# Kernel tuning notes

Measured on AMD Instinct MI355X. Metric: run time of the kernel, lower is better.

## Reference

```python
import jax, jax.numpy as jnp
import numpy as np

EPS = 1e-5


def _conv1x1(x, w, b=None):
    # x: [B,Cin,H,W], w: [Cout,Cin]
    y = jnp.einsum('bchw,oc->bohw', x, w)
    return y if b is None else y + b[None, :, None, None]


def _bn(x, g, bt, m, v):
    # inference-mode BatchNorm2d
    s = g / jnp.sqrt(v + EPS)
    return x * s[None, :, None, None] + (bt - m * s)[None, :, None, None]


def _emb(x, p):
    h = jax.nn.gelu(_conv1x1(x, p['emb_w1'], p['emb_b1']), approximate=False)
    return _conv1x1(h, p['emb_w2'], p['emb_b2'])  # dropout is identity in eval


def _forward(x0, x1, p):
    b, c, h, w = x0.shape
    hw = h * w
    half = c // 2
    xs = [x0, x1]
    la_res = None
    for k in range(4):
        # residual refinement of each scale
        for i in range(2):
            r = _conv1x1(xs[i], p['rb_w1'], p['rb_b1'])
            r = jax.nn.relu(_bn(r, p['rb_bn_g'], p['rb_bn_b'], p['rb_bn_m'], p['rb_bn_v']))
            r = _conv1x1(r, p['rb_w2'], p['rb_b2'])
            xs[i] = jax.nn.relu(_bn(xs[i] + r, p['bn_g'], p['bn_b'], p['bn_m'], p['bn_v']))
        # build per-pixel query [b,hw,half,4] and value [b,hw,4,half]
        qs, vs = [], []
        for i in range(2):
            q = _bn(_conv1x1(xs[i], p['q_w'], p['q_b']), p['q_bn_g'], p['q_bn_b'], p['q_bn_m'], p['q_bn_v'])
            qs += [q[:, :half], q[:, half:]]
            v = _bn(_conv1x1(xs[i], p['v_w'], p['v_b']), p['v_bn_g'], p['v_bn_b'], p['v_bn_m'], p['v_bn_v'])
            vs += [v[:, :half], v[:, half:]]
        query = jnp.stack(qs, axis=1).reshape(b, 4, half, hw).transpose(0, 3, 2, 1)
        value = jnp.stack(vs, axis=1).reshape(b, 4, half, hw).transpose(0, 3, 1, 2)
        if k == 0:
            cat = jnp.concatenate(xs, axis=1)
            la_res = jax.nn.relu(_bn(_conv1x1(cat, p['cf_w'], p['cf_b']),
                                     p['cf_bn_g'], p['cf_bn_b'], p['cf_bn_m'], p['cf_bn_v']))
            la_res = _emb(la_res, p)
        refs = []
        for pref in ('k1', 'k2'):
            kk = _bn(_conv1x1(la_res, p[pref + '_w'], p[pref + '_b']),
                     p[pref + '_bn_g'], p[pref + '_bn_b'], p[pref + '_bn_m'], p[pref + '_bn_v'])
            kk = kk.reshape(b, half, hw).transpose(0, 2, 1)            # [b,hw,half]
            att = jax.nn.softmax(jnp.einsum('bnc,bncm->bnm', kk, query), axis=-1)  # [b,hw,4]
            ref = jnp.einsum('bnm,bnmc->bnc', att, value)               # [b,hw,half]
            refs.append(ref.transpose(0, 2, 1).reshape(b, half, h, w))
        la_res = _emb(jnp.concatenate(refs, axis=1), p)
    return la_res


def setup_inputs() -> dict:
    b, c, h, w = 16, 48, 128, 128
    half = c // 2
    ks = iter(jax.random.split(jax.random.key(0), 64))
    def nrm(shape, s=1.0):
        return s * jax.random.normal(next(ks), shape, jnp.float32)
    inp = {'x0': nrm((b, c, h, w)), 'x1': nrm((b, c, h, w))}
    def conv(wn, bname, o, i):
        inp[wn] = nrm((o, i), 1.0 / np.sqrt(i))
        inp[bname] = nrm((o,), 0.02)
    def bnp(pref, n):
        inp[pref + '_g'] = 1.0 + nrm((n,), 0.1)
        inp[pref + '_b'] = nrm((n,), 0.1)
        inp[pref + '_m'] = nrm((n,), 0.1)
        inp[pref + '_v'] = 1.0 + 0.1 * jnp.abs(nrm((n,)))
    conv('rb_w1', 'rb_b1', half, c); bnp('rb_bn', half)
    conv('rb_w2', 'rb_b2', c, half); bnp('bn', c)
    conv('q_w', 'q_b', c, c); bnp('q_bn', c)
    conv('v_w', 'v_b', c, c); bnp('v_bn', c)
    conv('k1_w', 'k1_b', half, c); bnp('k1_bn', half)
    conv('k2_w', 'k2_b', half, c); bnp('k2_bn', half)
    conv('cf_w', 'cf_b', c, 2 * c); bnp('cf_bn', c)
    conv('emb_w1', 'emb_b1', half, c)
    conv('emb_w2', 'emb_b2', c, half)
    return inp


def reference(x0, x1, rb_w1, rb_b1, rb_bn_g, rb_bn_b, rb_bn_m, rb_bn_v, rb_w2, rb_b2,
              bn_g, bn_b, bn_m, bn_v, q_w, q_b, q_bn_g, q_bn_b, q_bn_m, q_bn_v,
              v_w, v_b, v_bn_g, v_bn_b, v_bn_m, v_bn_v,
              k1_w, k1_b, k1_bn_g, k1_bn_b, k1_bn_m, k1_bn_v,
              k2_w, k2_b, k2_bn_g, k2_bn_b, k2_bn_m, k2_bn_v,
              cf_w, cf_b, cf_bn_g, cf_bn_b, cf_bn_m, cf_bn_v,
              emb_w1, emb_b1, emb_w2, emb_b2):
    p = dict(rb_w1=rb_w1, rb_b1=rb_b1, rb_bn_g=rb_bn_g, rb_bn_b=rb_bn_b, rb_bn_m=rb_bn_m, rb_bn_v=rb_bn_v,
             rb_w2=rb_w2, rb_b2=rb_b2, bn_g=bn_g, bn_b=bn_b, bn_m=bn_m, bn_v=bn_v,
             q_w=q_w, q_b=q_b, q_bn_g=q_bn_g, q_bn_b=q_bn_b, q_bn_m=q_bn_m, q_bn_v=q_bn_v,
             v_w=v_w, v_b=v_b, v_bn_g=v_bn_g, v_bn_b=v_bn_b, v_bn_m=v_bn_m, v_bn_v=v_bn_v,
             k1_w=k1_w, k1_b=k1_b, k1_bn_g=k1_bn_g, k1_bn_b=k1_bn_b, k1_bn_m=k1_bn_m, k1_bn_v=k1_bn_v,
             k2_w=k2_w, k2_b=k2_b, k2_bn_g=k2_bn_g, k2_bn_b=k2_bn_b, k2_bn_m=k2_bn_m, k2_bn_v=k2_bn_v,
             cf_w=cf_w, cf_b=cf_b, cf_bn_g=cf_bn_g, cf_bn_b=cf_bn_b, cf_bn_m=cf_bn_m, cf_bn_v=cf_bn_v,
             emb_w1=emb_w1, emb_b1=emb_b1, emb_w2=emb_w2, emb_b2=emb_b2)
    return _forward(x0, x1, p)
```

## Files before the change

### kernel.cpp

```cpp
#include <hip/hip_runtime.h>
#include <hip/hip_fp16.h>
#include <stdint.h>
#include <math.h>

#define HWS 16384
#define NPIX (16 * HWS)
#define T 256

typedef _Float16 h2 __attribute__((ext_vector_type(2)));

enum {
  H_W1P = 0,
  F_B1  = 576,
  H_W2P = 600,
  F_B2  = 1176,
  F_XS  = 1224,
  H_M1A = 1272,
  H_M1B = 1848,
  H_M2A = 2424,
  H_M2B = 3000,
  F_C1A = 3576, F_C1B = 3624, F_C2A = 3672, F_C2B = 3720,
  F_D1A = 3768, F_D1B = 3792, F_D2A = 3816, F_D2B = 3840,
  F_E4  = 3864,
  H_P1  = 3868,
  H_P2  = 5020,
  F_Q1L = 6172, F_Q1H = 6196, F_Q2L = 6220, F_Q2H = 6244,
  F_BE1 = 6268,
  F_CFT = 6292,
  F_BCF = 10900,
  F_WE1 = 10948,
  F_BE2 = 12100,
  F_WE2R= 12148,
  WS_TOTAL = 13300
};

struct PtrPack { const float* p[48]; };

__device__ __forceinline__ void bnst(const PtrPack& P, int bnb, int o, float& s, float& t) {
  float g = P.p[bnb][o], be = P.p[bnb + 1][o], m = P.p[bnb + 2][o], v = P.p[bnb + 3][o];
  s = g / sqrtf(v + 1e-5f);
  t = be - m * s;
}
__device__ __forceinline__ float KFv(const PtrPack& P, const float* kw, int bnb, int ok, int j) {
  float s, t; bnst(P, bnb, ok, s, t);
  float a = 0.f;
  for (int cc = 0; cc < 48; cc++) a += kw[ok * 48 + cc] * P.p[46][cc * 24 + j];
  return s * a;
}
__device__ __forceinline__ float BFv(const PtrPack& P, const float* kw, const float* kb, int bnb, int ok) {
  float s, t; bnst(P, bnb, ok, s, t);
  float a = kb[ok];
  for (int cc = 0; cc < 48; cc++) a += kw[ok * 48 + cc] * P.p[47][cc];
  return s * a + t;
}
__device__ __forceinline__ float WQf(const PtrPack& P, int o, int c) { float s, t; bnst(P, 16, o, s, t); return s * P.p[14][o * 48 + c]; }
__device__ __forceinline__ float BQf(const PtrPack& P, int o) { float s, t; bnst(P, 16, o, s, t); return s * P.p[15][o] + t; }
__device__ __forceinline__ float WVf(const PtrPack& P, int o, int c) { float s, t; bnst(P, 22, o, s, t); return s * P.p[20][o * 48 + c]; }
__device__ __forceinline__ float BVf(const PtrPack& P, int o) { float s, t; bnst(P, 22, o, s, t); return s * P.p[21][o] + t; }

__device__ float w1v(const PtrPack& P, int c, int o) { float s, t; bnst(P, 4, o, s, t); return s * P.p[2][o * 48 + c]; }
__device__ float w2v(const PtrPack& P, int o, int c) { float s, t; bnst(P, 10, o, s, t); return s * P.p[8][o * 24 + c]; }
__device__ float m_v(const PtrPack& P, int which, int c, int j) {
  float a = 0.f;
  if (which == 0)      for (int ok = 0; ok < 24; ok++) a += KFv(P, P.p[26], 28, ok, j) * WQf(P, ok, c);
  else if (which == 1) for (int ok = 0; ok < 24; ok++) a += KFv(P, P.p[26], 28, ok, j) * WQf(P, 24 + ok, c);
  else if (which == 2) for (int ok = 0; ok < 24; ok++) a += KFv(P, P.p[32], 34, ok, j) * WQf(P, ok, c);
  else                 for (int ok = 0; ok < 24; ok++) a += KFv(P, P.p[32], 34, ok, j) * WQf(P, 24 + ok, c);
  return a;
}
__device__ float p_v(const PtrPack& P, int which, int c, int o) {
  float a = 0.f;
  if (which == 0)      for (int jj = 0; jj < 24; jj++) a += P.p[44][o * 48 + jj] * WVf(P, jj, c);
  else if (which == 1) for (int jj = 0; jj < 24; jj++) a += P.p[44][o * 48 + jj] * WVf(P, 24 + jj, c);
  else if (which == 2) for (int jj = 0; jj < 24; jj++) a += P.p[44][o * 48 + 24 + jj] * WVf(P, jj, c);
  else                 for (int jj = 0; jj < 24; jj++) a += P.p[44][o * 48 + 24 + jj] * WVf(P, 24 + jj, c);
  return a;
}

__device__ __forceinline__ float packh2(float a, float b) {
  __half2 h = __floats2half2_rn(a, b);
  union { __half2 h; float f; } x; x.h = h; return x.f;
}

__global__ void fold_kernel(PtrPack P, float* __restrict__ W) {
  int i = blockIdx.x * blockDim.x + threadIdx.x;
  if (i >= WS_TOTAL) return;
  float s, t, a;
  if (i < F_B1)        { int cp = i / 24, o = i % 24; W[i] = packh2(w1v(P, 2 * cp, o), w1v(P, 2 * cp + 1, o)); }
  else if (i < H_W2P)  { int o = i - F_B1; bnst(P, 4, o, s, t); W[i] = s * P.p[3][o] + t; }
  else if (i < F_B2)   { int j = i - H_W2P; int o = j / 12, cj = j % 12; W[i] = packh2(w2v(P, o, 2 * cj), w2v(P, o, 2 * cj + 1)); }
  else if (i < F_XS)   { int o = i - F_B2; bnst(P, 10, o, s, t); W[i] = s * P.p[9][o] + t; }
  else if (i < H_M1A)  { int o = i - F_XS; bnst(P, 10, o, s, t); W[i] = s; }
  else if (i < H_M1B)  { int j = i - H_M1A; int c = j / 12, jp = j % 12; W[i] = packh2(m_v(P, 0, c, 2 * jp), m_v(P, 0, c, 2 * jp + 1)); }
  else if (i < H_M2A)  { int j = i - H_M1B; int c = j / 12, jp = j % 12; W[i] = packh2(m_v(P, 1, c, 2 * jp), m_v(P, 1, c, 2 * jp + 1)); }
  else if (i < H_M2B)  { int j = i - H_M2A; int c = j / 12, jp = j % 12; W[i] = packh2(m_v(P, 2, c, 2 * jp), m_v(P, 2, c, 2 * jp + 1)); }
  else if (i < F_C1A)  { int j = i - H_M2B; int c = j / 12, jp = j % 12; W[i] = packh2(m_v(P, 3, c, 2 * jp), m_v(P, 3, c, 2 * jp + 1)); }
  else if (i < F_C1B)  { int c = i - F_C1A; a = 0.f; for (int ok = 0; ok < 24; ok++) a += BFv(P, P.p[26], P.p[27], 28, ok) * WQf(P, ok, c); W[i] = a; }
  else if (i < F_C2A)  { int c = i - F_C1B; a = 0.f; for (int ok = 0; ok < 24; ok++) a += BFv(P, P.p[26], P.p[27], 28, ok) * WQf(P, 24 + ok, c); W[i] = a; }
  else if (i < F_C2B)  { int c = i - F_C2A; a = 0.f; for (int ok = 0; ok < 24; ok++) a += BFv(P, P.p[32], P.p[33], 34, ok) * WQf(P, ok, c); W[i] = a; }
  else if (i < F_D1A)  { int c = i - F_C2B; a = 0.f; for (int ok = 0; ok < 24; ok++) a += BFv(P, P.p[32], P.p[33], 34, ok) * WQf(P, 24 + ok, c); W[i] = a; }
  else if (i < F_D1B)  { int j = i - F_D1A; a = 0.f; for (int ok = 0; ok < 24; ok++) a += KFv(P, P.p[26], 28, ok, j) * BQf(P, ok); W[i] = a; }
  else if (i < F_D2A)  { int j = i - F_D1B; a = 0.f; for (int ok = 0; ok < 24; ok++) a += KFv(P, P.p[26], 28, ok, j) * BQf(P, 24 + ok); W[i] = a; }
  else if (i < F_D2B)  { int j = i - F_D2A; a = 0.f; for (int ok = 0; ok < 24; ok++) a += KFv(P, P.p[32], 34, ok, j) * BQf(P, ok); W[i] = a; }
  else if (i < F_E4)   { int j = i - F_D2B; a = 0.f; for (int ok = 0; ok < 24; ok++) a += KFv(P, P.p[32], 34, ok, j) * BQf(P, 24 + ok); W[i] = a; }
  else if (i < H_P1)   { int e = i - F_E4; a = 0.f;
    if (e == 0)      for (int ok = 0; ok < 24; ok++) a += BFv(P, P.p[26], P.p[27], 28, ok) * BQf(P, ok);
    else if (e == 1) for (int ok = 0; ok < 24; ok++) a += BFv(P, P.p[26], P.p[27], 28, ok) * BQf(P, 24 + ok);
    else if (e == 2) for (int ok = 0; ok < 24; ok++) a += BFv(P, P.p[32], P.p[33], 34, ok) * BQf(P, ok);
    else             for (int ok = 0; ok < 24; ok++) a += BFv(P, P.p[32], P.p[33], 34, ok) * BQf(P, 24 + ok);
    W[i] = a; }
  else if (i < H_P2)   { int j = i - H_P1; int c = j / 24, o = j % 24; W[i] = packh2(p_v(P, 0, c, o), p_v(P, 1, c, o)); }
  else if (i < F_Q1L)  { int j = i - H_P2; int c = j / 24, o = j % 24; W[i] = packh2(p_v(P, 2, c, o), p_v(P, 3, c, o)); }
  else if (i < F_Q1H)  { int o = i - F_Q1L; a = 0.f; for (int jj = 0; jj < 24; jj++) a += P.p[44][o * 48 + jj] * BVf(P, jj); W[i] = a; }
  else if (i < F_Q2L)  { int o = i - F_Q1H; a = 0.f; for (int jj = 0; jj < 24; jj++) a += P.p[44][o * 48 + jj] * BVf(P, 24 + jj); W[i] = a; }
  else if (i < F_Q2H)  { int o = i - F_Q2L; a = 0.f; for (int jj = 0; jj < 24; jj++) a += P.p[44][o * 48 + 24 + jj] * BVf(P, jj); W[i] = a; }
  else if (i < F_BE1)  { int o = i - F_Q2H; a = 0.f; for (int jj = 0; jj < 24; jj++) a += P.p[44][o * 48 + 24 + jj] * BVf(P, 24 + jj); W[i] = a; }
  else if (i < F_CFT)  { int o = i - F_BE1; W[i] = P.p[45][o]; }
  else if (i < F_BCF)  { int j = i - F_CFT; int cin = j / 48, o = j % 48; bnst(P, 40, o, s, t); W[i] = s * P.p[38][o * 96 + cin]; }
  else if (i < F_WE1)  { int o = i - F_BCF; bnst(P, 40, o, s, t); W[i] = s * P.p[39][o] + t; }
  else if (i < F_BE2)  { int j = i - F_WE1; W[i] = P.p[44][j]; }
  else if (i < F_WE2R) { int o = i - F_BE2; W[i] = P.p[47][o]; }
  else                 { int j = i - F_WE2R; W[i] = P.p[46][j]; }
}


__device__ __forceinline__ float gelu_f(float x) {
  return 0.5f * x * (1.f + erff(x * 0.70710678118654752440f));
}
__device__ __forceinline__ float fdot2f(h2 a, h2 b, float c) {
#if __has_builtin(__builtin_amdgcn_fdot2)
  return __builtin_amdgcn_fdot2(a, b, c, false);
#else
  return fmaf((float)a[0], (float)b[0], fmaf((float)a[1], (float)b[1], c));
#endif
}
__device__ __forceinline__ h2 ldh(const float* __restrict__ W, int off) {
  union { float f; h2 h; } u; u.f = W[off]; return u.h;
}
__device__ __forceinline__ h2 ash2(__half2 v) {
  union { __half2 a; h2 h; } u; u.a = v; return u.h;
}
__device__ __forceinline__ h2 pk(float a, float b) {
  return ash2(__floats2half2_rn(a, b));
}

__global__ __launch_bounds__(T)
void fused_main(const float* __restrict__ x0g,
                const float* __restrict__ x1g,
                const float* __restrict__ W,
                float* __restrict__ out) {
  __shared__ __half2 Xh[2][24][T];
  const int tid = threadIdx.x;
  const int p = blockIdx.x * T + tid;
  const int b = p >> 14;
  const int n = p & (HWS - 1);

  {
    const float* px0 = x0g + (size_t)b * 48 * HWS + n;
    const float* px1 = x1g + (size_t)b * 48 * HWS + n;
#pragma unroll 1
    for (int cp = 0; cp < 24; cp++) {
      Xh[0][cp][tid] = __floats2half2_rn(px0[(size_t)(2 * cp) * HWS], px0[(size_t)(2 * cp + 1) * HWS]);
      Xh[1][cp][tid] = __floats2half2_rn(px1[(size_t)(2 * cp) * HWS], px1[(size_t)(2 * cp + 1) * HWS]);
    }
  }

  float h[24];

#pragma unroll 1
  for (int k = 0; k < 4; k++) {
#pragma unroll 1
    for (int s = 0; s < 2; s++) {
      float r[24];
#pragma unroll
      for (int o = 0; o < 24; o++) r[o] = W[F_B1 + o];
#pragma unroll 2
      for (int cp = 0; cp < 24; cp++) {
        h2 xp = ash2(Xh[s][cp][tid]);
#pragma unroll
        for (int o = 0; o < 24; o++) r[o] = fdot2f(ldh(W, H_W1P + cp * 24 + o), xp, r[o]);
      }
#pragma unroll
      for (int o = 0; o < 24; o++) r[o] = fmaxf(r[o], 0.f);
      h2 rp[12];
#pragma unroll
      for (int j = 0; j < 12; j++) rp[j] = pk(r[2 * j], r[2 * j + 1]);

#pragma unroll 2
      for (int op = 0; op < 24; op++) {
        float a0 = W[F_B2 + 2 * op], a1 = W[F_B2 + 2 * op + 1];
#pragma unroll
        for (int cj = 0; cj < 12; cj++) a0 = fdot2f(ldh(W, H_W2P + (2 * op) * 12 + cj), rp[cj], a0);
#pragma unroll
        for (int cj = 0; cj < 12; cj++) a1 = fdot2f(ldh(W, H_W2P + (2 * op + 1) * 12 + cj), rp[cj], a1);
        __half2 u = Xh[s][op][tid];
        float n0 = fmaxf(fmaf(W[F_XS + 2 * op], __low2float(u), a0), 0.f);
        float n1 = fmaxf(fmaf(W[F_XS + 2 * op + 1], __high2float(u), a1), 0.f);
        Xh[s][op][tid] = __floats2half2_rn(n0, n1);
      }
    }

    if (k == 0) {
      float tv[48];
#pragma unroll
      for (int o = 0; o < 48; o++) tv[o] = W[F_BCF + o];
#pragma unroll 1
      for (int s = 0; s < 2; s++) {
#pragma unroll 1
        for (int cp = 0; cp < 24; cp++) {
          __half2 u = Xh[s][cp][tid];
          float x0c = __low2float(u), x1c = __high2float(u);
          const float* w0 = &W[F_CFT + (s * 48 + 2 * cp) * 48];
#pragma unroll
          for (int o = 0; o < 48; o++) tv[o] = fmaf(w0[o], x0c, tv[o]);
#pragma unroll
          for (int o = 0; o < 48; o++) tv[o] = fmaf(w0[48 + o], x1c, tv[o]);
        }
      }
#pragma unroll
      for (int o = 0; o < 48; o++) tv[o] = fmaxf(tv[o], 0.f);
#pragma unroll
      for (int o = 0; o < 24; o++) {
        float a = W[F_BE1 + o];
#pragma unroll
        for (int c = 0; c < 48; c++) a = fmaf(W[F_WE1 + o * 48 + c], tv[c], a);
        h[o] = gelu_f(a);
      }
    }

    float s1[4], s2[4];
    {
      float b1a = W[F_E4 + 0], b1b = W[F_E4 + 1], b2a = W[F_E4 + 2], b2b = W[F_E4 + 3];
#pragma unroll
      for (int j = 0; j < 24; j++) {
        b1a = fmaf(W[F_D1A + j], h[j], b1a);
        b1b = fmaf(W[F_D1B + j], h[j], b1b);
        b2a = fmaf(W[F_D2A + j], h[j], b2a);
        b2b = fmaf(W[F_D2B + j], h[j], b2b);
      }
      s1[0] = b1a; s1[2] = b1a; s1[1] = b1b; s1[3] = b1b;
      s2[0] = b2a; s2[2] = b2a; s2[1] = b2b; s2[3] = b2b;
    }
    h2 hp[12];
#pragma unroll
    for (int j = 0; j < 12; j++) hp[j] = pk(h[2 * j], h[2 * j + 1]);

#pragma unroll 2
    for (int cp = 0; cp < 24; cp++) {
      __half2 u0 = Xh[0][cp][tid], u1 = Xh[1][cp][tid];
#pragma unroll
      for (int ch = 0; ch < 2; ch++) {
        int c = 2 * cp + ch;
        float z1a = W[F_C1A + c], z1b = W[F_C1B + c];
        float z2a = W[F_C2A + c], z2b = W[F_C2B + c];
#pragma unroll
        for (int jp = 0; jp < 12; jp++) {
          z1a = fdot2f(ldh(W, H_M1A + c * 12 + jp), hp[jp], z1a);
          z1b = fdot2f(ldh(W, H_M1B + c * 12 + jp), hp[jp], z1b);
          z2a = fdot2f(ldh(W, H_M2A + c * 12 + jp), hp[jp], z2a);
          z2b = fdot2f(ldh(W, H_M2B + c * 12 + jp), hp[jp], z2b);
        }
        float x0 = ch ? __high2float(u0) : __low2float(u0);
        float x1 = ch ? __high2float(u1) : __low2float(u1);
        s1[0] = fmaf(x0, z1a, s1[0]); s1[1] = fmaf(x0, z1b, s1[1]);
        s1[2] = fmaf(x1, z1a, s1[2]); s1[3] = fmaf(x1, z1b, s1[3]);
        s2[0] = fmaf(x0, z2a, s2[0]); s2[1] = fmaf(x0, z2b, s2[1]);
        s2[2] = fmaf(x1, z2a, s2[2]); s2[3] = fmaf(x1, z2b, s2[3]);
      }
    }
    {
      float m1 = fmaxf(fmaxf(s1[0], s1[1]), fmaxf(s1[2], s1[3]));
      float e0 = __expf(s1[0] - m1), e1 = __expf(s1[1] - m1), e2 = __expf(s1[2] - m1), e3 = __expf(s1[3] - m1);
      float inv = 1.f / (e0 + e1 + e2 + e3);
      s1[0] = e0 * inv; s1[1] = e1 * inv; s1[2] = e2 * inv; s1[3] = e3 * inv;
      float m2 = fmaxf(fmaxf(s2[0], s2[1]), fmaxf(s2[2], s2[3]));
      float f0 = __expf(s2[0] - m2), f1 = __expf(s2[1] - m2), f2 = __expf(s2[2] - m2), f3 = __expf(s2[3] - m2);
      float jnv = 1.f / (f0 + f1 + f2 + f3);
      s2[0] = f0 * jnv; s2[1] = f1 * jnv; s2[2] = f2 * jnv; s2[3] = f3 * jnv;
    }

    float hv[24];
    {
      float q1l = s1[0] + s1[2], q1h = s1[1] + s1[3];
      float q2l = s2[0] + s2[2], q2h = s2[1] + s2[3];
#pragma unroll
      for (int o = 0; o < 24; o++) {
        float a = W[F_BE1 + o];
        a = fmaf(q1l, W[F_Q1L + o], a);
        a = fmaf(q1h, W[F_Q1H + o], a);
        a = fmaf(q2l, W[F_Q2L + o], a);
        a = fmaf(q2h, W[F_Q2H + o], a);
        hv[o] = a;
      }
    }
#pragma unroll 2
    for (int cp = 0; cp < 24; cp++) {
      __half2 u0 = Xh[0][cp][tid], u1 = Xh[1][cp][tid];
#pragma unroll
      for (int ch = 0; ch < 2; ch++) {
        int c = 2 * cp + ch;
        float x0 = ch ? __high2float(u0) : __low2float(u0);
        float x1 = ch ? __high2float(u1) : __low2float(u1);
        float cA = fmaf(s1[0], x0, s1[2] * x1);
        float cB = fmaf(s1[1], x0, s1[3] * x1);
        float cC = fmaf(s2[0], x0, s2[2] * x1);
        float cD = fmaf(s2[1], x0, s2[3] * x1);
        h2 pAB = pk(cA, cB), pCD = pk(cC, cD);
#pragma unroll
        for (int o = 0; o < 24; o++) {
          float a = hv[o];
          a = fdot2f(ldh(W, H_P1 + c * 24 + o), pAB, a);
          a = fdot2f(ldh(W, H_P2 + c * 24 + o), pCD, a);
          hv[o] = a;
        }
      }
    }
#pragma unroll
    for (int o = 0; o < 24; o++) h[o] = gelu_f(hv[o]);
  }

  float* po = out + (size_t)b * 48 * HWS + n;
#pragma unroll 1
  for (int op = 0; op < 24; op++) {
    const float* w0 = &W[F_WE2R + (2 * op) * 24];
    float a0 = W[F_BE2 + 2 * op], a1 = W[F_BE2 + 2 * op + 1];
#pragma unroll
    for (int j = 0; j < 24; j++) a0 = fmaf(w0[j], h[j], a0);
#pragma unroll
    for (int j = 0; j < 24; j++) a1 = fmaf(w0[24 + j], h[j], a1);
    po[(size_t)(2 * op) * HWS] = a0;
    po[(size_t)(2 * op + 1) * HWS] = a1;
  }
}

extern "C" void kernel_launch(void* const* d_in, const int* in_sizes, int n_in,
                              void* d_out, int out_size, void* d_ws, size_t ws_size,
                              hipStream_t stream) {
  PtrPack P;
  for (int i = 0; i < 48; i++) P.p[i] = (const float*)d_in[i];
  float* W = (float*)d_ws;

  fold_kernel<<<(WS_TOTAL + 255) / 256, 256, 0, stream>>>(P, W);
  fused_main<<<NPIX / T, T, 0, stream>>>(P.p[0], P.p[1], W, (float*)d_out);
}
```

Measured before the change: 571.5 us.

## Repack folded weights into aligned rows and load them as per-lane 128-bit vectors

Rearranges the folded weight workspace so each row's weights, biases and scales sit together in 16-byte-aligned groups. All weight reads in the main kernel are routed through a pointer forced into vector registers, so they become dwordx4 global loads rather than scalar loads. This aims to cut scalar-load instruction count and waits and to reduce SGPR pressure. In exchange it adds vector memory traffic for data that is uniform across lanes, and it lowers some unroll factors.

```diff
diff --git a/kernel.cpp b/kernel.cpp
--- a/kernel.cpp
+++ b/kernel.cpp
@@ -8,30 +8,24 @@
 #define T 256
 
 typedef _Float16 h2 __attribute__((ext_vector_type(2)));
+typedef float f4v __attribute__((ext_vector_type(4)));
+union U4 { f4v v; float f[4]; h2 h[4]; };
 
 enum {
   H_W1P = 0,
   F_B1  = 576,
-  H_W2P = 600,
-  F_B2  = 1176,
-  F_XS  = 1224,
-  H_M1A = 1272,
-  H_M1B = 1848,
-  H_M2A = 2424,
-  H_M2B = 3000,
-  F_C1A = 3576, F_C1B = 3624, F_C2A = 3672, F_C2B = 3720,
-  F_D1A = 3768, F_D1B = 3792, F_D2A = 3816, F_D2B = 3840,
+  H_RB2 = 600,
+  H_SC  = 1272,
+  F_D4  = 3768,
   F_E4  = 3864,
-  H_P1  = 3868,
-  H_P2  = 5020,
-  F_Q1L = 6172, F_Q1H = 6196, F_Q2L = 6220, F_Q2H = 6244,
+  H_PV  = 3868,
+  F_Q4  = 6172,
   F_BE1 = 6268,
   F_CFT = 6292,
   F_BCF = 10900,
   F_WE1 = 10948,
-  F_BE2 = 12100,
-  F_WE2R= 12148,
-  WS_TOTAL = 13300
+  F_WE2 = 12100,
+  WS_TOTAL = 13348
 };
 
 struct PtrPack { const float* p[48]; };
@@ -76,6 +70,38 @@
   else                 for (int jj = 0; jj < 24; jj++) a += P.p[44][o * 48 + 24 + jj] * WVf(P, 24 + jj, c);
   return a;
 }
+__device__ float c_v(const PtrPack& P, int e, int c) {
+  float a = 0.f;
+  if (e == 0)      for (int ok = 0; ok < 24; ok++) a += BFv(P, P.p[26], P.p[27], 28, ok) * WQf(P, ok, c);
+  else if (e == 1) for (int ok = 0; ok < 24; ok++) a += BFv(P, P.p[26], P.p[27], 28, ok) * WQf(P, 24 + ok, c);
+  else if (e == 2) for (int ok = 0; ok < 24; ok++) a += BFv(P, P.p[32], P.p[33], 34, ok) * WQf(P, ok, c);
+  else             for (int ok = 0; ok < 24; ok++) a += BFv(P, P.p[32], P.p[33], 34, ok) * WQf(P, 24 + ok, c);
+  return a;
+}
+__device__ float d_v(const PtrPack& P, int e, int j) {
+  float a = 0.f;
+  if (e == 0)      for (int ok = 0; ok < 24; ok++) a += KFv(P, P.p[26], 28, ok, j) * BQf(P, ok);
+  else if (e == 1) for (int ok = 0; ok < 24; ok++) a += KFv(P, P.p[26], 28, ok, j) * BQf(P, 24 + ok);
+  else if (e == 2) for (int ok = 0; ok < 24; ok++) a += KFv(P, P.p[32], 34, ok, j) * BQf(P, ok);
+  else             for (int ok = 0; ok < 24; ok++) a += KFv(P, P.p[32], 34, ok, j) * BQf(P, 24 + ok);
+  return a;
+}
+__device__ float e_v(const PtrPack& P, int e) {
+  float a = 0.f;
+  if (e == 0)      for (int ok = 0; ok < 24; ok++) a += BFv(P, P.p[26], P.p[27], 28, ok) * BQf(P, ok);
+  else if (e == 1) for (int ok = 0; ok < 24; ok++) a += BFv(P, P.p[26], P.p[27], 28, ok) * BQf(P, 24 + ok);
+  else if (e == 2) for (int ok = 0; ok < 24; ok++) a += BFv(P, P.p[32], P.p[33], 34, ok) * BQf(P, ok);
+  else             for (int ok = 0; ok < 24; ok++) a += BFv(P, P.p[32], P.p[33], 34, ok) * BQf(P, 24 + ok);
+  return a;
+}
+__device__ float q_v(const PtrPack& P, int e, int o) {
+  float a = 0.f;
+  if (e == 0)      for (int jj = 0; jj < 24; jj++) a += P.p[44][o * 48 + jj] * BVf(P, jj);
+  else if (e == 1) for (int jj = 0; jj < 24; jj++) a += P.p[44][o * 48 + jj] * BVf(P, 24 + jj);
+  else if (e == 2) for (int jj = 0; jj < 24; jj++) a += P.p[44][o * 48 + 24 + jj] * BVf(P, jj);
+  else             for (int jj = 0; jj < 24; jj++) a += P.p[44][o * 48 + 24 + jj] * BVf(P, 24 + jj);
+  return a;
+}
 
 __device__ __forceinline__ float packh2(float a, float b) {
   __half2 h = __floats2half2_rn(a, b);
@@ -85,42 +111,47 @@
 __global__ void fold_kernel(PtrPack P, float* __restrict__ W) {
   int i = blockIdx.x * blockDim.x + threadIdx.x;
   if (i >= WS_TOTAL) return;
-  float s, t, a;
-  if (i < F_B1)        { int cp = i / 24, o = i % 24; W[i] = packh2(w1v(P, 2 * cp, o), w1v(P, 2 * cp + 1, o)); }
-  else if (i < H_W2P)  { int o = i - F_B1; bnst(P, 4, o, s, t); W[i] = s * P.p[3][o] + t; }
-  else if (i < F_B2)   { int j = i - H_W2P; int o = j / 12, cj = j % 12; W[i] = packh2(w2v(P, o, 2 * cj), w2v(P, o, 2 * cj + 1)); }
-  else if (i < F_XS)   { int o = i - F_B2; bnst(P, 10, o, s, t); W[i] = s * P.p[9][o] + t; }
-  else if (i < H_M1A)  { int o = i - F_XS; bnst(P, 10, o, s, t); W[i] = s; }
-  else if (i < H_M1B)  { int j = i - H_M1A; int c = j / 12, jp = j % 12; W[i] = packh2(m_v(P, 0, c, 2 * jp), m_v(P, 0, c, 2 * jp + 1)); }
-  else if (i < H_M2A)  { int j = i - H_M1B; int c = j / 12, jp = j % 12; W[i] = packh2(m_v(P, 1, c, 2 * jp), m_v(P, 1, c, 2 * jp + 1)); }
-  else if (i < H_M2B)  { int j = i - H_M2A; int c = j / 12, jp = j % 12; W[i] = packh2(m_v(P, 2, c, 2 * jp), m_v(P, 2, c, 2 * jp + 1)); }
-  else if (i < F_C1A)  { int j = i - H_M2B; int c = j / 12, jp = j % 12; W[i] = packh2(m_v(P, 3, c, 2 * jp), m_v(P, 3, c, 2 * jp + 1)); }
-  else if (i < F_C1B)  { int c = i - F_C1A; a = 0.f; for (int ok = 0; ok < 24; ok++) a += BFv(P, P.p[26], P.p[27], 28, ok) * WQf(P, ok, c); W[i] = a; }
-  else if (i < F_C2A)  { int c = i - F_C1B; a = 0.f; for (int ok = 0; ok < 24; ok++) a += BFv(P, P.p[26], P.p[27], 28, ok) * WQf(P, 24 + ok, c); W[i] = a; }
-  else if (i < F_C2B)  { int c = i - F_C2A; a = 0.f; for (int ok = 0; ok < 24; ok++) a += BFv(P, P.p[32], P.p[33], 34, ok) * WQf(P, ok, c); W[i] = a; }
-  else if (i < F_D1A)  { int c = i - F_C2B; a = 0.f; for (int ok = 0; ok < 24; ok++) a += BFv(P, P.p[32], P.p[33], 34, ok) * WQf(P, 24 + ok, c); W[i] = a; }
-  else if (i < F_D1B)  { int j = i - F_D1A; a = 0.f; for (int ok = 0; ok < 24; ok++) a += KFv(P, P.p[26], 28, ok, j) * BQf(P, ok); W[i] = a; }
-  else if (i < F_D2A)  { int j = i - F_D1B; a = 0.f; for (int ok = 0; ok < 24; ok++) a += KFv(P, P.p[26], 28, ok, j) * BQf(P, 24 + ok); W[i] = a; }
-  else if (i < F_D2B)  { int j = i - F_D2A; a = 0.f; for (int ok = 0; ok < 24; ok++) a += KFv(P, P.p[32], 34, ok, j) * BQf(P, ok); W[i] = a; }
-  else if (i < F_E4)   { int j = i - F_D2B; a = 0.f; for (int ok = 0; ok < 24; ok++) a += KFv(P, P.p[32], 34, ok, j) * BQf(P, 24 + ok); W[i] = a; }
-  else if (i < H_P1)   { int e = i - F_E4; a = 0.f;
-    if (e == 0)      for (int ok = 0; ok < 24; ok++) a += BFv(P, P.p[26], P.p[27], 28, ok) * BQf(P, ok);
-    else if (e == 1) for (int ok = 0; ok < 24; ok++) a += BFv(P, P.p[26], P.p[27], 28, ok) * BQf(P, 24 + ok);
-    else if (e == 2) for (int ok = 0; ok < 24; ok++) a += BFv(P, P.p[32], P.p[33], 34, ok) * BQf(P, ok);
-    else             for (int ok = 0; ok < 24; ok++) a += BFv(P, P.p[32], P.p[33], 34, ok) * BQf(P, 24 + ok);
-    W[i] = a; }
-  else if (i < H_P2)   { int j = i - H_P1; int c = j / 24, o = j % 24; W[i] = packh2(p_v(P, 0, c, o), p_v(P, 1, c, o)); }
-  else if (i < F_Q1L)  { int j = i - H_P2; int c = j / 24, o = j % 24; W[i] = packh2(p_v(P, 2, c, o), p_v(P, 3, c, o)); }
-  else if (i < F_Q1H)  { int o = i - F_Q1L; a = 0.f; for (int jj = 0; jj < 24; jj++) a += P.p[44][o * 48 + jj] * BVf(P, jj); W[i] = a; }
-  else if (i < F_Q2L)  { int o = i - F_Q1H; a = 0.f; for (int jj = 0; jj < 24; jj++) a += P.p[44][o * 48 + jj] * BVf(P, 24 + jj); W[i] = a; }
-  else if (i < F_Q2H)  { int o = i - F_Q2L; a = 0.f; for (int jj = 0; jj < 24; jj++) a += P.p[44][o * 48 + 24 + jj] * BVf(P, jj); W[i] = a; }
-  else if (i < F_BE1)  { int o = i - F_Q2H; a = 0.f; for (int jj = 0; jj < 24; jj++) a += P.p[44][o * 48 + 24 + jj] * BVf(P, 24 + jj); W[i] = a; }
-  else if (i < F_CFT)  { int o = i - F_BE1; W[i] = P.p[45][o]; }
-  else if (i < F_BCF)  { int j = i - F_CFT; int cin = j / 48, o = j % 48; bnst(P, 40, o, s, t); W[i] = s * P.p[38][o * 96 + cin]; }
-  else if (i < F_WE1)  { int o = i - F_BCF; bnst(P, 40, o, s, t); W[i] = s * P.p[39][o] + t; }
-  else if (i < F_BE2)  { int j = i - F_WE1; W[i] = P.p[44][j]; }
-  else if (i < F_WE2R) { int o = i - F_BE2; W[i] = P.p[47][o]; }
-  else                 { int j = i - F_WE2R; W[i] = P.p[46][j]; }
+  float s, t;
+  if (i < F_B1) { int cp = i / 24, o = i % 24; W[i] = packh2(w1v(P, 2 * cp, o), w1v(P, 2 * cp + 1, o)); }
+  else if (i < H_RB2) { int o = i - F_B1; bnst(P, 4, o, s, t); W[i] = s * P.p[3][o] + t; }
+  else if (i < H_SC) {
+    int j = i - H_RB2; int op = j / 28, r = j % 28;
+    if (r < 12)       W[i] = packh2(w2v(P, 2 * op, 2 * r), w2v(P, 2 * op, 2 * r + 1));
+    else if (r < 24)  { int rr = r - 12; W[i] = packh2(w2v(P, 2 * op + 1, 2 * rr), w2v(P, 2 * op + 1, 2 * rr + 1)); }
+    else {
+      int e = r - 24; int o2 = 2 * op + (e & 1);
+      bnst(P, 10, o2, s, t);
+      W[i] = (e < 2) ? (s * P.p[9][o2] + t) : s;
+    }
+  }
+  else if (i < F_D4) {
+    int j = i - H_SC; int c = j / 52, r = j % 52;
+    if (r < 12)       W[i] = packh2(m_v(P, 0, c, 2 * r), m_v(P, 0, c, 2 * r + 1));
+    else if (r < 24)  { int rr = r - 12; W[i] = packh2(m_v(P, 1, c, 2 * rr), m_v(P, 1, c, 2 * rr + 1)); }
+    else if (r < 36)  { int rr = r - 24; W[i] = packh2(m_v(P, 2, c, 2 * rr), m_v(P, 2, c, 2 * rr + 1)); }
+    else if (r < 48)  { int rr = r - 36; W[i] = packh2(m_v(P, 3, c, 2 * rr), m_v(P, 3, c, 2 * rr + 1)); }
+    else              W[i] = c_v(P, r - 48, c);
+  }
+  else if (i < F_E4) { int j = i - F_D4; W[i] = d_v(P, j % 4, j / 4); }
+  else if (i < H_PV) { W[i] = e_v(P, i - F_E4); }
+  else if (i < F_Q4) {
+    int j = i - H_PV; int c = j / 48, r = j % 48;
+    if (r < 24) W[i] = packh2(p_v(P, 0, c, r), p_v(P, 1, c, r));
+    else        { int rr = r - 24; W[i] = packh2(p_v(P, 2, c, rr), p_v(P, 3, c, rr)); }
+  }
+  else if (i < F_BE1) { int j = i - F_Q4; W[i] = q_v(P, j % 4, j / 4); }
+  else if (i < F_CFT) { W[i] = P.p[45][i - F_BE1]; }
+  else if (i < F_BCF) { int j = i - F_CFT; int cin = j / 48, o = j % 48; bnst(P, 40, o, s, t); W[i] = s * P.p[38][o * 96 + cin]; }
+  else if (i < F_WE1) { int o = i - F_BCF; bnst(P, 40, o, s, t); W[i] = s * P.p[39][o] + t; }
+  else if (i < F_WE2) { W[i] = P.p[44][i - F_WE1]; }
+  else {
+    int j = i - F_WE2; int op = j / 52, r = j % 52;
+    if (r < 24)       W[i] = P.p[46][(2 * op) * 24 + r];
+    else if (r < 48)  W[i] = P.p[46][(2 * op + 1) * 24 + (r - 24)];
+    else if (r == 48) W[i] = P.p[47][2 * op];
+    else if (r == 49) W[i] = P.p[47][2 * op + 1];
+    else              W[i] = 0.f;
+  }
 }
 
 
@@ -134,14 +165,17 @@
   return fmaf((float)a[0], (float)b[0], fmaf((float)a[1], (float)b[1], c));
 #endif
 }
-__device__ __forceinline__ h2 ldh(const float* __restrict__ W, int off) {
-  union { float f; h2 h; } u; u.f = W[off]; return u.h;
-}
 __device__ __forceinline__ h2 ash2(__half2 v) {
   union { __half2 a; h2 h; } u; u.a = v; return u.h;
 }
 __device__ __forceinline__ h2 pk(float a, float b) {
   return ash2(__floats2half2_rn(a, b));
+}
+typedef const __attribute__((address_space(1))) f4v* gf4p;
+__device__ __forceinline__ gf4p vrow(const float* W, int off) {
+  unsigned long long a = (unsigned long long)(W + off);
+  asm("" : "+v"(a));
+  return (gf4p)a;
 }
 
 __global__ __launch_bounds__(T)
@@ -172,13 +206,26 @@
 #pragma unroll 1
     for (int s = 0; s < 2; s++) {
       float r[24];
-#pragma unroll
-      for (int o = 0; o < 24; o++) r[o] = W[F_B1 + o];
+      {
+        gf4p pb = vrow(W, F_B1);
+#pragma unroll
+        for (int q = 0; q < 6; q++) {
+          U4 bq; bq.v = pb[q];
+          r[4 * q] = bq.f[0]; r[4 * q + 1] = bq.f[1]; r[4 * q + 2] = bq.f[2]; r[4 * q + 3] = bq.f[3];
+        }
+      }
 #pragma unroll 2
       for (int cp = 0; cp < 24; cp++) {
         h2 xp = ash2(Xh[s][cp][tid]);
-#pragma unroll
-        for (int o = 0; o < 24; o++) r[o] = fdot2f(ldh(W, H_W1P + cp * 24 + o), xp, r[o]);
+        gf4p pw = vrow(W, H_W1P + cp * 24);
+#pragma unroll
+        for (int q = 0; q < 6; q++) {
+          U4 w; w.v = pw[q];
+          r[4 * q]     = fdot2f(w.h[0], xp, r[4 * q]);
+          r[4 * q + 1] = fdot2f(w.h[1], xp, r[4 * q + 1]);
+          r[4 * q + 2] = fdot2f(w.h[2], xp, r[4 * q + 2]);
+          r[4 * q + 3] = fdot2f(w.h[3], xp, r[4 * q + 3]);
+        }
       }
 #pragma unroll
       for (int o = 0; o < 24; o++) r[o] = fmaxf(r[o], 0.f);
@@ -188,55 +235,84 @@
 
 #pragma unroll 2
       for (int op = 0; op < 24; op++) {
-        float a0 = W[F_B2 + 2 * op], a1 = W[F_B2 + 2 * op + 1];
-#pragma unroll
-        for (int cj = 0; cj < 12; cj++) a0 = fdot2f(ldh(W, H_W2P + (2 * op) * 12 + cj), rp[cj], a0);
-#pragma unroll
-        for (int cj = 0; cj < 12; cj++) a1 = fdot2f(ldh(W, H_W2P + (2 * op + 1) * 12 + cj), rp[cj], a1);
+        gf4p pw = vrow(W, H_RB2 + op * 28);
+        U4 bx; bx.v = pw[6];
+        float a0 = bx.f[0], a1 = bx.f[1];
+#pragma unroll
+        for (int q = 0; q < 3; q++) {
+          U4 w; w.v = pw[q];
+#pragma unroll
+          for (int e = 0; e < 4; e++) a0 = fdot2f(w.h[e], rp[4 * q + e], a0);
+        }
+#pragma unroll
+        for (int q = 0; q < 3; q++) {
+          U4 w; w.v = pw[3 + q];
+#pragma unroll
+          for (int e = 0; e < 4; e++) a1 = fdot2f(w.h[e], rp[4 * q + e], a1);
+        }
         __half2 u = Xh[s][op][tid];
-        float n0 = fmaxf(fmaf(W[F_XS + 2 * op], __low2float(u), a0), 0.f);
-        float n1 = fmaxf(fmaf(W[F_XS + 2 * op + 1], __high2float(u), a1), 0.f);
+        float n0 = fmaxf(fmaf(bx.f[2], __low2float(u), a0), 0.f);
+        float n1 = fmaxf(fmaf(bx.f[3], __high2float(u), a1), 0.f);
         Xh[s][op][tid] = __floats2half2_rn(n0, n1);
       }
     }
 
     if (k == 0) {
       float tv[48];
-#pragma unroll
-      for (int o = 0; o < 48; o++) tv[o] = W[F_BCF + o];
+      {
+        gf4p pb = vrow(W, F_BCF);
+#pragma unroll
+        for (int q = 0; q < 12; q++) {
+          U4 bq; bq.v = pb[q];
+#pragma unroll
+          for (int e = 0; e < 4; e++) tv[4 * q + e] = bq.f[e];
+        }
+      }
 #pragma unroll 1
       for (int s = 0; s < 2; s++) {
 #pragma unroll 1
         for (int cp = 0; cp < 24; cp++) {
           __half2 u = Xh[s][cp][tid];
           float x0c = __low2float(u), x1c = __high2float(u);
-          const float* w0 = &W[F_CFT + (s * 48 + 2 * cp) * 48];
-#pragma unroll
-          for (int o = 0; o < 48; o++) tv[o] = fmaf(w0[o], x0c, tv[o]);
-#pragma unroll
-          for (int o = 0; o < 48; o++) tv[o] = fmaf(w0[48 + o], x1c, tv[o]);
+          gf4p wa = vrow(W, F_CFT + (s * 48 + 2 * cp) * 48);
+          gf4p wb = vrow(W, F_CFT + (s * 48 + 2 * cp + 1) * 48);
+#pragma unroll
+          for (int q = 0; q < 12; q++) {
+            U4 a; a.v = wa[q];
+            U4 bq; bq.v = wb[q];
+#pragma unroll
+            for (int e = 0; e < 4; e++) tv[4 * q + e] = fmaf(a.f[e], x0c, fmaf(bq.f[e], x1c, tv[4 * q + e]));
+          }
         }
       }
 #pragma unroll
       for (int o = 0; o < 48; o++) tv[o] = fmaxf(tv[o], 0.f);
-#pragma unroll
+#pragma unroll 2
       for (int o = 0; o < 24; o++) {
+        gf4p pw = vrow(W, F_WE1 + o * 48);
         float a = W[F_BE1 + o];
 #pragma unroll
-        for (int c = 0; c < 48; c++) a = fmaf(W[F_WE1 + o * 48 + c], tv[c], a);
+        for (int q = 0; q < 12; q++) {
+          U4 w; w.v = pw[q];
+#pragma unroll
+          for (int e = 0; e < 4; e++) a = fmaf(w.f[e], tv[4 * q + e], a);
+        }
         h[o] = gelu_f(a);
       }
     }
 
     float s1[4], s2[4];
     {
-      float b1a = W[F_E4 + 0], b1b = W[F_E4 + 1], b2a = W[F_E4 + 2], b2b = W[F_E4 + 3];
+      U4 e4; e4.v = *vrow(W, F_E4);
+      float b1a = e4.f[0], b1b = e4.f[1], b2a = e4.f[2], b2b = e4.f[3];
+      gf4p pd = vrow(W, F_D4);
 #pragma unroll
       for (int j = 0; j < 24; j++) {
-        b1a = fmaf(W[F_D1A + j], h[j], b1a);
-        b1b = fmaf(W[F_D1B + j], h[j], b1b);
-        b2a = fmaf(W[F_D2A + j], h[j], b2a);
-        b2b = fmaf(W[F_D2B + j], h[j], b2b);
+        U4 d; d.v = pd[j];
+        b1a = fmaf(d.f[0], h[j], b1a);
+        b1b = fmaf(d.f[1], h[j], b1b);
+        b2a = fmaf(d.f[2], h[j], b2a);
+        b2b = fmaf(d.f[3], h[j], b2b);
       }
       s1[0] = b1a; s1[2] = b1a; s1[1] = b1b; s1[3] = b1b;
       s2[0] = b2a; s2[2] = b2a; s2[1] = b2b; s2[3] = b2b;
@@ -245,20 +321,38 @@
 #pragma unroll
     for (int j = 0; j < 12; j++) hp[j] = pk(h[2 * j], h[2 * j + 1]);
 
-#pragma unroll 2
+#pragma unroll 1
     for (int cp = 0; cp < 24; cp++) {
       __half2 u0 = Xh[0][cp][tid], u1 = Xh[1][cp][tid];
 #pragma unroll
       for (int ch = 0; ch < 2; ch++) {
         int c = 2 * cp + ch;
-        float z1a = W[F_C1A + c], z1b = W[F_C1B + c];
-        float z2a = W[F_C2A + c], z2b = W[F_C2B + c];
-#pragma unroll
-        for (int jp = 0; jp < 12; jp++) {
-          z1a = fdot2f(ldh(W, H_M1A + c * 12 + jp), hp[jp], z1a);
-          z1b = fdot2f(ldh(W, H_M1B + c * 12 + jp), hp[jp], z1b);
-          z2a = fdot2f(ldh(W, H_M2A + c * 12 + jp), hp[jp], z2a);
-          z2b = fdot2f(ldh(W, H_M2B + c * 12 + jp), hp[jp], z2b);
+        gf4p pm = vrow(W, H_SC + c * 52);
+        U4 cc; cc.v = pm[12];
+        float z1a = cc.f[0], z1b = cc.f[1], z2a = cc.f[2], z2b = cc.f[3];
+#pragma unroll
+        for (int q = 0; q < 3; q++) {
+          U4 w; w.v = pm[q];
+#pragma unroll
+          for (int e = 0; e < 4; e++) z1a = fdot2f(w.h[e], hp[4 * q + e], z1a);
+        }
+#pragma unroll
+        for (int q = 0; q < 3; q++) {
+          U4 w; w.v = pm[3 + q];
+#pragma unroll
+          for (int e = 0; e < 4; e++) z1b = fdot2f(w.h[e], hp[4 * q + e], z1b);
+        }
+#pragma unroll
+        for (int q = 0; q < 3; q++) {
+          U4 w; w.v = pm[6 + q];
+#pragma unroll
+          for (int e = 0; e < 4; e++) z2a = fdot2f(w.h[e], hp[4 * q + e], z2a);
+        }
+#pragma unroll
+        for (int q = 0; q < 3; q++) {
+          U4 w; w.v = pm[9 + q];
+#pragma unroll
+          for (int e = 0; e < 4; e++) z2b = fdot2f(w.h[e], hp[4 * q + e], z2b);
         }
         float x0 = ch ? __high2float(u0) : __low2float(u0);
         float x1 = ch ? __high2float(u1) : __low2float(u1);
@@ -283,17 +377,20 @@
     {
       float q1l = s1[0] + s1[2], q1h = s1[1] + s1[3];
       float q2l = s2[0] + s2[2], q2h = s2[1] + s2[3];
-#pragma unroll
-      for (int o = 0; o < 24; o++) {
-        float a = W[F_BE1 + o];
-        a = fmaf(q1l, W[F_Q1L + o], a);
-        a = fmaf(q1h, W[F_Q1H + o], a);
-        a = fmaf(q2l, W[F_Q2L + o], a);
-        a = fmaf(q2h, W[F_Q2H + o], a);
-        hv[o] = a;
-      }
-    }
-#pragma unroll 2
+      gf4p pq = vrow(W, F_Q4);
+      gf4p pb = vrow(W, F_BE1);
+#pragma unroll
+      for (int g = 0; g < 6; g++) {
+        U4 bq; bq.v = pb[g];
+#pragma unroll
+        for (int e = 0; e < 4; e++) {
+          int o = 4 * g + e;
+          U4 qq; qq.v = pq[o];
+          hv[o] = fmaf(q1l, qq.f[0], fmaf(q1h, qq.f[1], fmaf(q2l, qq.f[2], fmaf(q2h, qq.f[3], bq.f[e]))));
+        }
+      }
+    }
+#pragma unroll 1
     for (int cp = 0; cp < 24; cp++) {
       __half2 u0 = Xh[0][cp][tid], u1 = Xh[1][cp][tid];
 #pragma unroll
@@ -306,12 +403,18 @@
         float cC = fmaf(s2[0], x0, s2[2] * x1);
         float cD = fmaf(s2[1], x0, s2[3] * x1);
         h2 pAB = pk(cA, cB), pCD = pk(cC, cD);
-#pragma unroll
-        for (int o = 0; o < 24; o++) {
-          float a = hv[o];
-          a = fdot2f(ldh(W, H_P1 + c * 24 + o), pAB, a);
-          a = fdot2f(ldh(W, H_P2 + c * 24 + o), pCD, a);
-          hv[o] = a;
+        gf4p pp = vrow(W, H_PV + c * 48);
+#pragma unroll
+        for (int q = 0; q < 6; q++) {
+          U4 w; w.v = pp[q];
+#pragma unroll
+          for (int e = 0; e < 4; e++) hv[4 * q + e] = fdot2f(w.h[e], pAB, hv[4 * q + e]);
+        }
+#pragma unroll
+        for (int q = 0; q < 6; q++) {
+          U4 w; w.v = pp[6 + q];
+#pragma unroll
+          for (int e = 0; e < 4; e++) hv[4 * q + e] = fdot2f(w.h[e], pCD, hv[4 * q + e]);
         }
       }
     }
@@ -322,12 +425,21 @@
   float* po = out + (size_t)b * 48 * HWS + n;
 #pragma unroll 1
   for (int op = 0; op < 24; op++) {
-    const float* w0 = &W[F_WE2R + (2 * op) * 24];
-    float a0 = W[F_BE2 + 2 * op], a1 = W[F_BE2 + 2 * op + 1];
-#pragma unroll
-    for (int j = 0; j < 24; j++) a0 = fmaf(w0[j], h[j], a0);
-#pragma unroll
-    for (int j = 0; j < 24; j++) a1 = fmaf(w0[24 + j], h[j], a1);
+    gf4p pw = vrow(W, F_WE2 + op * 52);
+    U4 bx; bx.v = pw[12];
+    float a0 = bx.f[0], a1 = bx.f[1];
+#pragma unroll
+    for (int q = 0; q < 6; q++) {
+      U4 w; w.v = pw[q];
+#pragma unroll
+      for (int e = 0; e < 4; e++) a0 = fmaf(w.f[e], h[4 * q + e], a0);
+    }
+#pragma unroll
+    for (int q = 0; q < 6; q++) {
+      U4 w; w.v = pw[6 + q];
+#pragma unroll
+      for (int e = 0; e < 4; e++) a1 = fmaf(w.f[e], h[4 * q + e], a1);
+    }
     po[(size_t)(2 * op) * HWS] = a0;
     po[(size_t)(2 * op + 1) * HWS] = a1;
   }
```

Result: slower. 1.432 ms (+150.6%).
